# Performance work log

Hardware: AMD Instinct MI355X
Metric: run time of the kernel (lower is better)

Reference implementation:

```python
import jax, jax.numpy as jnp
import numpy as np

B, S, D, H, FF = 2, 2048, 1024, 16, 4096
DH = D // H  # per-head dim = 64
EPS = 1e-5


def layer_norm(x, g, b):
    mu = jnp.mean(x, axis=-1, keepdims=True)
    var = jnp.mean((x - mu) ** 2, axis=-1, keepdims=True)
    return (x - mu) * jax.lax.rsqrt(var + EPS) * g + b


def setup_inputs() -> dict:
    key = jax.random.key(0)
    ks = jax.random.split(key, 12)
    s_in = 1.0 / np.sqrt(D)
    s_ff = 1.0 / np.sqrt(FF)
    return {
        "x": jax.random.normal(ks[0], (B, S, D), jnp.float32),
        # per-head projections stacked over heads: [H, D, DH]
        "Wq": jax.random.normal(ks[1], (H, D, DH), jnp.float32) * s_in,
        "bq": jnp.zeros((H, DH), jnp.float32),
        "Wk": jax.random.normal(ks[2], (H, D, DH), jnp.float32) * s_in,
        "bk": jnp.zeros((H, DH), jnp.float32),
        "Wv": jax.random.normal(ks[3], (H, D, DH), jnp.float32) * s_in,
        "bv": jnp.zeros((H, DH), jnp.float32),
        "ln1_g": jnp.ones((D,), jnp.float32),
        "ln1_b": jnp.zeros((D,), jnp.float32),
        "ln2_g": jnp.ones((D,), jnp.float32),
        "ln2_b": jnp.zeros((D,), jnp.float32),
        "W1": jax.random.normal(ks[4], (D, FF), jnp.float32) * s_in,
        "b1": jnp.zeros((FF,), jnp.float32),
        "W2": jax.random.normal(ks[5], (FF, D), jnp.float32) * s_ff,
        "b2": jnp.zeros((D,), jnp.float32),
    }


def reference(x, Wq, bq, Wk, bk, Wv, bv, ln1_g, ln1_b, ln2_g, ln2_b, W1, b1, W2, b2):
    # --- attention sub-block (pre-LN) ---
    h = layer_norm(x, ln1_g, ln1_b)                      # [B,S,D]
    q = jnp.einsum('bsd,hde->bhse', h, Wq) + bq[None, :, None, :]
    k = jnp.einsum('bsd,hde->bhse', h, Wk) + bk[None, :, None, :]
    v = jnp.einsum('bsd,hde->bhse', h, Wv) + bv[None, :, None, :]
    score = jnp.einsum('bhse,bhte->bhst', q, k) / jnp.sqrt(jnp.float32(DH))
    causal = jnp.tril(jnp.ones((S, S), bool))            # lower-triangular mask
    score = jnp.where(causal, score, -jnp.inf)
    attn = jax.nn.softmax(score, axis=-1)                # [B,H,S,S]
    o = jnp.einsum('bhst,bhte->bhse', attn, v)           # [B,H,S,DH]
    o = jnp.transpose(o, (0, 2, 1, 3)).reshape(B, S, D)  # concat heads
    x = x + o
    # --- FFN sub-block (pre-LN) ---
    h2 = layer_norm(x, ln2_g, ln2_b)
    f = jax.nn.gelu(h2 @ W1 + b1, approximate=False) @ W2 + b2
    return x + f
```

## Files before the change

### kernel.cpp

```cpp
#include <hip/hip_runtime.h>
#include <hip/hip_bf16.h>
#include <cstdint>
#include <cstddef>


typedef short bf16x8 __attribute__((ext_vector_type(8)));
typedef float f32x4 __attribute__((ext_vector_type(4)));

#define DEV static __device__ __forceinline__

DEV unsigned short f2bf(float f) {
  union { float fv; unsigned u; } a; a.fv = f;
  unsigned r = a.u + 0x7FFFu + ((a.u >> 16) & 1u);
  return (unsigned short)(r >> 16);
}

DEV void gload_lds16(const void* g, void* l) {
  __builtin_amdgcn_global_load_lds(
      (const __attribute__((address_space(1))) unsigned int*)g,
      (__attribute__((address_space(3))) unsigned int*)l,
      16, 0, 0);
}

__global__ __launch_bounds__(256) void k_transpose(const float* __restrict__ in,
                                                   unsigned short* __restrict__ out,
                                                   int R, int C,
                                                   long inBatchStride, long outBatchStride) {
  __shared__ float tile[32][33];
  long batch = blockIdx.z;
  int c0 = blockIdx.x * 32;
  int r0 = blockIdx.y * 32;
  const float* src = in + batch * inBatchStride;
  unsigned short* dst = out + batch * outBatchStride;
  int tx = threadIdx.x, ty = threadIdx.y;
  #pragma unroll
  for (int i = ty; i < 32; i += 8)
    tile[i][tx] = src[(long)(r0 + i) * C + (c0 + tx)];
  __syncthreads();
  #pragma unroll
  for (int i = ty; i < 32; i += 8)
    dst[(long)(c0 + i) * R + (r0 + tx)] = f2bf(tile[tx][i]);
}

__global__ void k_concat_bias(const float* __restrict__ bq, const float* __restrict__ bk,
                              const float* __restrict__ bv, float* __restrict__ out) {
  int i = blockIdx.x * 256 + threadIdx.x;
  if (i < 1024) out[i] = bq[i];
  else if (i < 2048) out[i] = bk[i - 1024];
  else if (i < 3072) out[i] = bv[i - 2048];
}

__global__ __launch_bounds__(256) void k_ln_bf16(const float* __restrict__ x,
                                                 const float* __restrict__ g,
                                                 const float* __restrict__ b,
                                                 unsigned short* __restrict__ out) {
  int row = blockIdx.x;
  const float* xr = x + (size_t)row * 1024;
  int t = threadIdx.x;
  float4 v = *(const float4*)(xr + t * 4);
  float s = v.x + v.y + v.z + v.w;
  float s2 = v.x * v.x + v.y * v.y + v.z * v.z + v.w * v.w;
  for (int off = 32; off > 0; off >>= 1) {
    s  += __shfl_down(s,  off, 64);
    s2 += __shfl_down(s2, off, 64);
  }
  __shared__ float ws1[4], ws2[4];
  __shared__ float mu_s, rs_s;
  int wid = t >> 6, lane = t & 63;
  if (lane == 0) { ws1[wid] = s; ws2[wid] = s2; }
  __syncthreads();
  if (t == 0) {
    float S1 = ws1[0] + ws1[1] + ws1[2] + ws1[3];
    float S2 = ws2[0] + ws2[1] + ws2[2] + ws2[3];
    float mu = S1 * (1.0f / 1024.0f);
    float var = S2 * (1.0f / 1024.0f) - mu * mu;
    mu_s = mu;
    rs_s = rsqrtf(var + 1e-5f);
  }
  __syncthreads();
  float mu = mu_s, rs = rs_s;
  float4 gv = *(const float4*)(g + t * 4);
  float4 bv = *(const float4*)(b + t * 4);
  ushort4 o;
  o.x = f2bf((v.x - mu) * rs * gv.x + bv.x);
  o.y = f2bf((v.y - mu) * rs * gv.y + bv.y);
  o.z = f2bf((v.z - mu) * rs * gv.z + bv.z);
  o.w = f2bf((v.w - mu) * rs * gv.w + bv.w);
  *(ushort4*)(out + (size_t)row * 1024 + t * 4) = o;
}

template <int EPI>
__global__ __launch_bounds__(256) void k_gemm_bt(const unsigned short* __restrict__ A,
                                                 const unsigned short* __restrict__ Bt,
                                                 const float* __restrict__ bias,
                                                 void* __restrict__ Cout,
                                                 int M, int N, int K) {
  __shared__ __align__(16) unsigned short As[128 * 64];
  __shared__ __align__(16) unsigned short Bs[128 * 64];
  int tid = threadIdx.x;
  int col0 = blockIdx.x * 128;
  int row0 = blockIdx.y * 128;
  int wid = tid >> 6, lane = tid & 63;
  int wr = wid >> 1, wc = wid & 1;
  int lrow = lane & 15;
  int kgrp = (lane >> 4) * 8;
  int srow = tid >> 3;
  int scol = (tid & 7) * 8;

  f32x4 acc[4][4];
  f32x4 zero = {0.f, 0.f, 0.f, 0.f};
  #pragma unroll
  for (int m = 0; m < 4; ++m)
    #pragma unroll
    for (int n = 0; n < 4; ++n) acc[m][n] = zero;

  for (int k0 = 0; k0 < K; k0 += 64) {
    #pragma unroll
    for (int i = 0; i < 4; ++i) {
      int r = i * 32 + srow;
      gload_lds16(A  + (size_t)(row0 + r) * K + k0 + scol, (char*)As + i * 4096 + tid * 16);
      gload_lds16(Bt + (size_t)(col0 + r) * K + k0 + scol, (char*)Bs + i * 4096 + tid * 16);
    }
    __syncthreads();
    bf16x8 af[4][2], bf[4][2];
    #pragma unroll
    for (int m = 0; m < 4; ++m)
      #pragma unroll
      for (int kk = 0; kk < 2; ++kk)
        af[m][kk] = *(const bf16x8*)(As + (wr * 64 + m * 16 + lrow) * 64 + kk * 32 + kgrp);
    #pragma unroll
    for (int n = 0; n < 4; ++n)
      #pragma unroll
      for (int kk = 0; kk < 2; ++kk)
        bf[n][kk] = *(const bf16x8*)(Bs + (wc * 64 + n * 16 + lrow) * 64 + kk * 32 + kgrp);
    #pragma unroll
    for (int m = 0; m < 4; ++m)
      #pragma unroll
      for (int n = 0; n < 4; ++n)
        #pragma unroll
        for (int kk = 0; kk < 2; ++kk)
          acc[m][n] = __builtin_amdgcn_mfma_f32_16x16x32_bf16(af[m][kk], bf[n][kk], acc[m][n], 0, 0, 0);
    __syncthreads();
  }

  int rbase = row0 + wr * 64 + (lane >> 4) * 4;
  int cbase = col0 + wc * 64 + (lane & 15);
  #pragma unroll
  for (int m = 0; m < 4; ++m) {
    #pragma unroll
    for (int n = 0; n < 4; ++n) {
      int col = cbase + n * 16;
      float bia = bias[col];
      #pragma unroll
      for (int j = 0; j < 4; ++j) {
        int row = rbase + m * 16 + j;
        float v = acc[m][n][j] + bia;
        if constexpr (EPI == 0) {
          ((unsigned short*)Cout)[(size_t)row * N + col] = f2bf(v);
        } else if constexpr (EPI == 1) {
          float gel = 0.5f * v * (1.0f + erff(v * 0.70710678118f));
          ((unsigned short*)Cout)[(size_t)row * N + col] = f2bf(gel);
        } else {
          float* o = (float*)Cout + (size_t)row * N + col;
          *o += v;
        }
      }
    }
  }
}

__global__ __launch_bounds__(256) void k_flash_attn(const unsigned short* __restrict__ qkv,
                                                    const float* __restrict__ x,
                                                    float* __restrict__ out) {
  int blk = blockIdx.x;
  int pairIdx = blk & 15;
  int bh = blk >> 4;
  int b = bh >> 4, h = bh & 15;
  const int LDQ = 3072;
  int tb = b * 2048;
  int qcol = h * 64, kcol = 1024 + h * 64, vcol = 2048 + h * 64;
  int tid = threadIdx.x, wid = tid >> 6, lane = tid & 63;
  int lrow = lane & 15;
  int g = lane >> 4;
  int kgrp = g * 8;

  __shared__ __align__(16) unsigned short Ks[2][64 * 64];
  __shared__ __align__(16) unsigned short Vt[2][64 * 64];
  __shared__ __align__(16) unsigned short Pl[4][16 * 64];

  int s_row = tid >> 3;
  int s_srccol = ((tid & 7) ^ ((tid >> 3) & 7)) * 8;

  unsigned short* myP = &Pl[wid][0];
  f32x4 zero = {0.f, 0.f, 0.f, 0.f};

  for (int half = 0; half < 2; ++half) {
    int qt = (half == 0) ? pairIdx : 31 - pairIdx;
    int q0 = qt * 64;
    int nkv = qt + 1;

    bf16x8 aq[2];
    #pragma unroll
    for (int kk = 0; kk < 2; ++kk)
      aq[kk] = *(const bf16x8*)(qkv + (size_t)(tb + q0 + wid * 16 + lrow) * LDQ + qcol + kk * 32 + kgrp);

    f32x4 oacc[4];
    #pragma unroll
    for (int e = 0; e < 4; ++e) oacc[e] = zero;
    float mrun[4], lrun[4];
    #pragma unroll
    for (int r = 0; r < 4; ++r) { mrun[r] = -1e30f; lrun[r] = 0.0f; }

    int cur = 0;
    bf16x8 vreg[2];

    #pragma unroll
    for (int i = 0; i < 2; ++i)
      gload_lds16(qkv + (size_t)(tb + i * 32 + s_row) * LDQ + kcol + s_srccol,
                  (char*)Ks[0] + i * 4096 + tid * 16);
    #pragma unroll
    for (int i = 0; i < 2; ++i) {
      int chunk = i * 256 + tid;
      vreg[i] = *(const bf16x8*)(qkv + (size_t)(tb + (chunk >> 3)) * LDQ + vcol + (chunk & 7) * 8);
    }
    #pragma unroll
    for (int i = 0; i < 2; ++i) {
      int chunk = i * 256 + tid;
      int t = chunk >> 3, e0 = (chunk & 7) * 8;
      #pragma unroll
      for (int jj = 0; jj < 8; ++jj) {
        int e = e0 + jj;
        int byteoff = e * 128 + ((((t >> 3) ^ (e & 7) ^ (e >> 3)) & 7) << 4) + (t & 7) * 2;
        *(unsigned short*)((char*)Vt[0] + byteoff) = (unsigned short)vreg[i][jj];
      }
    }

    for (int j = 0; j < nkv; ++j) {
      __syncthreads();
      int nxt = cur ^ 1;
      bool pf = (j + 1 < nkv);
      if (pf) {
        #pragma unroll
        for (int i = 0; i < 2; ++i)
          gload_lds16(qkv + (size_t)(tb + (j + 1) * 64 + i * 32 + s_row) * LDQ + kcol + s_srccol,
                      (char*)Ks[nxt] + i * 4096 + tid * 16);
        #pragma unroll
        for (int i = 0; i < 2; ++i) {
          int chunk = i * 256 + tid;
          vreg[i] = *(const bf16x8*)(qkv + (size_t)(tb + (j + 1) * 64 + (chunk >> 3)) * LDQ + vcol + (chunk & 7) * 8);
        }
      }

      f32x4 sacc[4];
      #pragma unroll
      for (int n = 0; n < 4; ++n) sacc[n] = zero;
      #pragma unroll
      for (int n = 0; n < 4; ++n) {
        int trow = n * 16 + lrow;
        #pragma unroll
        for (int kk = 0; kk < 2; ++kk) {
          int byteoff = trow * 128 + (((kk * 4 + g) ^ (trow & 7)) << 4);
          bf16x8 bk = *(const bf16x8*)((const char*)Ks[cur] + byteoff);
          sacc[n] = __builtin_amdgcn_mfma_f32_16x16x32_bf16(aq[kk], bk, sacc[n], 0, 0, 0);
        }
      }

      bool diag = (j == qt);
      float pv[4][4];
      #pragma unroll
      for (int r = 0; r < 4; ++r) {
        int sg = q0 + wid * 16 + g * 4 + r;
        float mx = -1e30f;
        #pragma unroll
        for (int n = 0; n < 4; ++n) {
          float sv = sacc[n][r] * 0.125f;
          int tg = j * 64 + n * 16 + lrow;
          if (diag && tg > sg) sv = -1e30f;
          pv[r][n] = sv;
          mx = fmaxf(mx, sv);
        }
        #pragma unroll
        for (int off = 1; off < 16; off <<= 1) mx = fmaxf(mx, __shfl_xor(mx, off, 64));
        float mnew = fmaxf(mrun[r], mx);
        float esc = __expf(mrun[r] - mnew);
        float rsum = 0.f;
        #pragma unroll
        for (int n = 0; n < 4; ++n) {
          float p = __expf(pv[r][n] - mnew);
          pv[r][n] = p;
          rsum += p;
        }
        #pragma unroll
        for (int off = 1; off < 16; off <<= 1) rsum += __shfl_xor(rsum, off, 64);
        lrun[r] = lrun[r] * esc + rsum;
        mrun[r] = mnew;
        #pragma unroll
        for (int e = 0; e < 4; ++e) oacc[e][r] *= esc;
      }

      if (pf) {
        #pragma unroll
        for (int i = 0; i < 2; ++i) {
          int chunk = i * 256 + tid;
          int t = chunk >> 3, e0 = (chunk & 7) * 8;
          #pragma unroll
          for (int jj = 0; jj < 8; ++jj) {
            int e = e0 + jj;
            int byteoff = e * 128 + ((((t >> 3) ^ (e & 7) ^ (e >> 3)) & 7) << 4) + (t & 7) * 2;
            *(unsigned short*)((char*)Vt[nxt] + byteoff) = (unsigned short)vreg[i][jj];
          }
        }
      }

      #pragma unroll
      for (int r = 0; r < 4; ++r) {
        int q = g * 4 + r;
        #pragma unroll
        for (int n = 0; n < 4; ++n) {
          int t = n * 16 + lrow;
          int byteoff = q * 128 + ((((t >> 3) ^ (q & 7)) & 7) << 4) + (t & 7) * 2;
          *(unsigned short*)((char*)myP + byteoff) = f2bf(pv[r][n]);
        }
      }

      #pragma unroll
      for (int kk = 0; kk < 2; ++kk) {
        int pbyte = lrow * 128 + (((kk * 4 + g) ^ (lrow & 7)) << 4);
        bf16x8 ap = *(const bf16x8*)((const char*)myP + pbyte);
        #pragma unroll
        for (int e = 0; e < 4; ++e) {
          int erow = e * 16 + lrow;
          int vbyte = erow * 128 + ((((kk * 4 + g) ^ (erow & 7) ^ (erow >> 3)) & 7) << 4);
          bf16x8 bv = *(const bf16x8*)((const char*)Vt[cur] + vbyte);
          oacc[e] = __builtin_amdgcn_mfma_f32_16x16x32_bf16(ap, bv, oacc[e], 0, 0, 0);
        }
      }
      cur = nxt;
    }

    #pragma unroll
    for (int r = 0; r < 4; ++r) {
      float inv = 1.0f / lrun[r];
      int row = tb + q0 + wid * 16 + g * 4 + r;
      #pragma unroll
      for (int e = 0; e < 4; ++e) {
        size_t idx = (size_t)row * 1024 + h * 64 + e * 16 + lrow;
        out[idx] = x[idx] + oacc[e][r] * inv;
      }
    }
  }
}

extern "C" void kernel_launch(void* const* d_in, const int* in_sizes, int n_in,
                              void* d_out, int out_size, void* d_ws, size_t ws_size,
                              hipStream_t stream) {
  (void)in_sizes; (void)n_in; (void)out_size; (void)ws_size;
  const float* x    = (const float*)d_in[0];
  const float* Wq   = (const float*)d_in[1];
  const float* bq   = (const float*)d_in[2];
  const float* Wk   = (const float*)d_in[3];
  const float* bk   = (const float*)d_in[4];
  const float* Wv   = (const float*)d_in[5];
  const float* bv   = (const float*)d_in[6];
  const float* ln1g = (const float*)d_in[7];
  const float* ln1b = (const float*)d_in[8];
  const float* ln2g = (const float*)d_in[9];
  const float* ln2b = (const float*)d_in[10];
  const float* W1   = (const float*)d_in[11];
  const float* b1   = (const float*)d_in[12];
  const float* W2   = (const float*)d_in[13];
  const float* b2   = (const float*)d_in[14];
  float* out = (float*)d_out;
  char* ws = (char*)d_ws;

  unsigned short* h1    = (unsigned short*)(ws + 0);
  unsigned short* wqkvT = (unsigned short*)(ws + 8388608);
  unsigned short* w1T   = (unsigned short*)(ws + 14680064);
  unsigned short* w2T   = (unsigned short*)(ws + 23068672);
  float*          bqkv  = (float*)(ws + 31457280);
  unsigned short* qkv   = (unsigned short*)(ws + 33554432);
  unsigned short* fbuf  = (unsigned short*)(ws + 33554432);

  dim3 tb(32, 8);
  k_transpose<<<dim3(2, 32, 16), tb, 0, stream>>>(Wq, wqkvT,               1024, 64, 1024L * 64, 64L * 1024);
  k_transpose<<<dim3(2, 32, 16), tb, 0, stream>>>(Wk, wqkvT + 1024 * 1024, 1024, 64, 1024L * 64, 64L * 1024);
  k_transpose<<<dim3(2, 32, 16), tb, 0, stream>>>(Wv, wqkvT + 2048 * 1024, 1024, 64, 1024L * 64, 64L * 1024);
  k_transpose<<<dim3(128, 32, 1), tb, 0, stream>>>(W1, w1T, 1024, 4096, 0, 0);
  k_transpose<<<dim3(32, 128, 1), tb, 0, stream>>>(W2, w2T, 4096, 1024, 0, 0);
  k_concat_bias<<<12, 256, 0, stream>>>(bq, bk, bv, bqkv);

  k_ln_bf16<<<4096, 256, 0, stream>>>(x, ln1g, ln1b, h1);
  k_gemm_bt<0><<<dim3(24, 32), 256, 0, stream>>>(h1, wqkvT, bqkv, qkv, 4096, 3072, 1024);
  k_flash_attn<<<512, 256, 0, stream>>>(qkv, x, out);
  k_ln_bf16<<<4096, 256, 0, stream>>>(out, ln2g, ln2b, h1);
  k_gemm_bt<1><<<dim3(32, 32), 256, 0, stream>>>(h1, w1T, b1, fbuf, 4096, 4096, 1024);
  k_gemm_bt<2><<<dim3(8, 32), 256, 0, stream>>>(fbuf, w2T, b2, out, 4096, 1024, 4096);
}
```

Measured before the change: 450.9 us.

## Swizzle GEMM LDS and workgroup order, split-K FFN2, raise MFMA priority in attention

The GEMM kernel now XOR-swizzles its LDS layout to avoid bank conflicts on fragment reads. It remaps the flat block index across 8 groups for XCD/L2 locality and adds a split-K option. The down-projection GEMM runs with two K parts and accumulates into the output with atomicAdd, which doubles its occupancy from 256 blocks. The flash-attention kernel wraps its MFMA sections in s_setprio to favour matrix issue. Atomic float accumulation makes the summation order nondeterministic and adds atomic traffic.

```diff
diff --git a/kernel.cpp b/kernel.cpp
--- a/kernel.cpp
+++ b/kernel.cpp
@@ -94,18 +94,30 @@
                                                  const unsigned short* __restrict__ Bt,
                                                  const float* __restrict__ bias,
                                                  void* __restrict__ Cout,
-                                                 int M, int N, int K) {
+                                                 int M, int N, int K,
+                                                 int nbx, int nby, int kparts) {
   __shared__ __align__(16) unsigned short As[128 * 64];
   __shared__ __align__(16) unsigned short Bs[128 * 64];
   int tid = threadIdx.x;
-  int col0 = blockIdx.x * 128;
-  int row0 = blockIdx.y * 128;
+
+  int nwg = nbx * nby * kparts;
+  int flat = blockIdx.x;
+  int swz = (flat & 7) * (nwg >> 3) + (flat >> 3);
+  int bx = swz % nbx;
+  int rest = swz / nbx;
+  int by = rest % nby;
+  int kp = rest / nby;
+  int col0 = bx * 128;
+  int row0 = by * 128;
+  int kLen = K / kparts;
+  int kBeg = kp * kLen;
+
   int wid = tid >> 6, lane = tid & 63;
   int wr = wid >> 1, wc = wid & 1;
   int lrow = lane & 15;
-  int kgrp = (lane >> 4) * 8;
-  int srow = tid >> 3;
-  int scol = (tid & 7) * 8;
+  int g = lane >> 4;
+  int s_row = tid >> 3;
+  int s_scol = ((tid & 7) ^ (s_row & 7)) * 8;
 
   f32x4 acc[4][4];
   f32x4 zero = {0.f, 0.f, 0.f, 0.f};
@@ -114,25 +126,33 @@
     #pragma unroll
     for (int n = 0; n < 4; ++n) acc[m][n] = zero;
 
-  for (int k0 = 0; k0 < K; k0 += 64) {
+  for (int k0 = kBeg; k0 < kBeg + kLen; k0 += 64) {
     #pragma unroll
     for (int i = 0; i < 4; ++i) {
-      int r = i * 32 + srow;
-      gload_lds16(A  + (size_t)(row0 + r) * K + k0 + scol, (char*)As + i * 4096 + tid * 16);
-      gload_lds16(Bt + (size_t)(col0 + r) * K + k0 + scol, (char*)Bs + i * 4096 + tid * 16);
+      int r = i * 32 + s_row;
+      gload_lds16(A  + (size_t)(row0 + r) * K + k0 + s_scol, (char*)As + i * 4096 + tid * 16);
+      gload_lds16(Bt + (size_t)(col0 + r) * K + k0 + s_scol, (char*)Bs + i * 4096 + tid * 16);
     }
     __syncthreads();
     bf16x8 af[4][2], bf[4][2];
     #pragma unroll
-    for (int m = 0; m < 4; ++m)
-      #pragma unroll
-      for (int kk = 0; kk < 2; ++kk)
-        af[m][kk] = *(const bf16x8*)(As + (wr * 64 + m * 16 + lrow) * 64 + kk * 32 + kgrp);
-    #pragma unroll
-    for (int n = 0; n < 4; ++n)
-      #pragma unroll
-      for (int kk = 0; kk < 2; ++kk)
-        bf[n][kk] = *(const bf16x8*)(Bs + (wc * 64 + n * 16 + lrow) * 64 + kk * 32 + kgrp);
+    for (int m = 0; m < 4; ++m) {
+      int ra = wr * 64 + m * 16 + lrow;
+      #pragma unroll
+      for (int kk = 0; kk < 2; ++kk) {
+        int byteoff = ra * 128 + (((kk * 4 + g) ^ (lrow & 7)) << 4);
+        af[m][kk] = *(const bf16x8*)((const char*)As + byteoff);
+      }
+    }
+    #pragma unroll
+    for (int n = 0; n < 4; ++n) {
+      int rb = wc * 64 + n * 16 + lrow;
+      #pragma unroll
+      for (int kk = 0; kk < 2; ++kk) {
+        int byteoff = rb * 128 + (((kk * 4 + g) ^ (lrow & 7)) << 4);
+        bf[n][kk] = *(const bf16x8*)((const char*)Bs + byteoff);
+      }
+    }
     #pragma unroll
     for (int m = 0; m < 4; ++m)
       #pragma unroll
@@ -143,8 +163,8 @@
     __syncthreads();
   }
 
-  int rbase = row0 + wr * 64 + (lane >> 4) * 4;
-  int cbase = col0 + wc * 64 + (lane & 15);
+  int rbase = row0 + wr * 64 + g * 4;
+  int cbase = col0 + wc * 64 + lrow;
   #pragma unroll
   for (int m = 0; m < 4; ++m) {
     #pragma unroll
@@ -154,15 +174,16 @@
       #pragma unroll
       for (int j = 0; j < 4; ++j) {
         int row = rbase + m * 16 + j;
-        float v = acc[m][n][j] + bia;
+        float v = acc[m][n][j];
         if constexpr (EPI == 0) {
-          ((unsigned short*)Cout)[(size_t)row * N + col] = f2bf(v);
+          ((unsigned short*)Cout)[(size_t)row * N + col] = f2bf(v + bia);
         } else if constexpr (EPI == 1) {
-          float gel = 0.5f * v * (1.0f + erff(v * 0.70710678118f));
+          float u = v + bia;
+          float gel = 0.5f * u * (1.0f + erff(u * 0.70710678118f));
           ((unsigned short*)Cout)[(size_t)row * N + col] = f2bf(gel);
         } else {
-          float* o = (float*)Cout + (size_t)row * N + col;
-          *o += v;
+          float u = v + (kp == 0 ? bia : 0.0f);
+          atomicAdd((float*)Cout + (size_t)row * N + col, u);
         }
       }
     }
@@ -254,6 +275,7 @@
       f32x4 sacc[4];
       #pragma unroll
       for (int n = 0; n < 4; ++n) sacc[n] = zero;
+      __builtin_amdgcn_s_setprio(1);
       #pragma unroll
       for (int n = 0; n < 4; ++n) {
         int trow = n * 16 + lrow;
@@ -264,6 +286,7 @@
           sacc[n] = __builtin_amdgcn_mfma_f32_16x16x32_bf16(aq[kk], bk, sacc[n], 0, 0, 0);
         }
       }
+      __builtin_amdgcn_s_setprio(0);
 
       bool diag = (j == qt);
       float pv[4][4];
@@ -323,6 +346,7 @@
         }
       }
 
+      __builtin_amdgcn_s_setprio(1);
       #pragma unroll
       for (int kk = 0; kk < 2; ++kk) {
         int pbyte = lrow * 128 + (((kk * 4 + g) ^ (lrow & 7)) << 4);
@@ -335,6 +359,7 @@
           oacc[e] = __builtin_amdgcn_mfma_f32_16x16x32_bf16(ap, bv, oacc[e], 0, 0, 0);
         }
       }
+      __builtin_amdgcn_s_setprio(0);
       cur = nxt;
     }
 
@@ -390,9 +415,9 @@
   k_concat_bias<<<12, 256, 0, stream>>>(bq, bk, bv, bqkv);
 
   k_ln_bf16<<<4096, 256, 0, stream>>>(x, ln1g, ln1b, h1);
-  k_gemm_bt<0><<<dim3(24, 32), 256, 0, stream>>>(h1, wqkvT, bqkv, qkv, 4096, 3072, 1024);
+  k_gemm_bt<0><<<768, 256, 0, stream>>>(h1, wqkvT, bqkv, qkv, 4096, 3072, 1024, 24, 32, 1);
   k_flash_attn<<<512, 256, 0, stream>>>(qkv, x, out);
   k_ln_bf16<<<4096, 256, 0, stream>>>(out, ln2g, ln2b, h1);
-  k_gemm_bt<1><<<dim3(32, 32), 256, 0, stream>>>(h1, w1T, b1, fbuf, 4096, 4096, 1024);
-  k_gemm_bt<2><<<dim3(8, 32), 256, 0, stream>>>(fbuf, w2T, b2, out, 4096, 1024, 4096);
-}
+  k_gemm_bt<1><<<1024, 256, 0, stream>>>(h1, w1T, b1, fbuf, 4096, 4096, 1024, 32, 32, 1);
+  k_gemm_bt<2><<<512, 256, 0, stream>>>(fbuf, w2T, b2, out, 4096, 1024, 4096, 8, 32, 2);
+}
```

After: 392.1 us. 13.0% less time.
